# Kernel tuning notes

Hardware: AMD Instinct MI355X
Metric: run time of the kernel (lower is better)

The kernel has to match this reference:

```python
import jax, jax.numpy as jnp
import numpy as np
from jax import lax

C_IN, C_OUT, H, W = 64, 128, 512, 512


def setup_inputs() -> dict:
    key = jax.random.key(0)
    k1, k2, k3, k4 = jax.random.split(key, 4)
    x = jax.random.normal(k1, (C_IN, H, W), dtype=jnp.float32)
    # Conv2d params (eqx default: kernel 3x3, bias used). Small init scale for stability.
    conv_w = jax.random.normal(k2, (C_OUT, C_IN, 3, 3), dtype=jnp.float32) * 0.05
    conv_b = jax.random.normal(k3, (C_OUT,), dtype=jnp.float32) * 0.05
    fft_mask = jax.random.normal(k4, (C_OUT, H, W), dtype=jnp.float32)
    return {"x": x, "conv_w": conv_w, "conv_b": conv_b, "fft_mask": fft_mask}


def reference(x, conv_w, conv_b, fft_mask):
    # 3x3 same-padding conv on a single (C,H,W) sample -> (C_OUT,H,W)
    y = lax.conv_general_dilated(
        x[None],  # (1,C_IN,H,W)
        conv_w,
        window_strides=(1, 1),
        padding=((1, 1), (1, 1)),
        dimension_numbers=("NCHW", "OIHW", "NCHW"),
    )[0] + conv_b[:, None, None]
    # Per-channel spectral filter: FFT over (H,W), elementwise complex-mask
    # multiply, inverse FFT, take real part. Vectorized over channels.
    Y = jnp.fft.fftn(y, axes=(1, 2)) * fft_mask
    return jnp.fft.ifftn(Y, axes=(1, 2)).real
```

## Files before the change

### kernel.cpp

```cpp
#include <hip/hip_runtime.h>

#define CIN   64
#define COUT  128
#define HH    512
#define WW    512
#define HW    (HH*WW)

typedef __attribute__((ext_vector_type(8))) short  short8;
typedef __attribute__((ext_vector_type(4))) float  floatx4;


__device__ __forceinline__ unsigned short f2bf(float f) {
    unsigned u = __float_as_uint(f);
    u += 0x7fffu + ((u >> 16) & 1u);
    return (unsigned short)(u >> 16);
}

__device__ __forceinline__ void wave_sync() {
    __builtin_amdgcn_wave_barrier();
    asm volatile("s_waitcnt lgkmcnt(0)" ::: "memory");
    __builtin_amdgcn_sched_barrier(0);
}
template<bool BLK> __device__ __forceinline__ void xsync() {
    if (BLK) __syncthreads(); else wave_sync();
}


__global__ __launch_bounds__(256) void k_wprep(
        const float* __restrict__ cw,
        unsigned short* __restrict__ wt)
{
    int i = blockIdx.x * 256 + threadIdx.x;
    int tap = i >> 13;
    int co  = (i >> 6) & 127;
    int ci  = i & 63;
    wt[i] = f2bf(cw[(co * 64 + ci) * 9 + tap]);
}


__global__ __launch_bounds__(256) void k_xprep(
        const float* __restrict__ x,
        unsigned short* __restrict__ xt)
{
    __shared__ unsigned short tile[64][72];
    int t  = threadIdx.x;
    int h  = blockIdx.x >> 3;
    int w0 = (blockIdx.x & 7) << 6;
    int wl = t & 63;
#pragma unroll
    for (int it = 0; it < 16; ++it) {
        int ci = (t >> 6) + 4 * it;
        tile[wl][ci] = f2bf(x[ci * HW + h * 512 + w0 + wl]);
    }
    __syncthreads();
#pragma unroll
    for (int it = 0; it < 2; ++it) {
        int task = t + 256 * it;
        int w = task >> 3, seg = task & 7;
        *(short8*)&xt[((size_t)(h * 512 + w0 + w)) * 64 + seg * 8] =
            *(const short8*)&tile[w][seg * 8];
    }
}


__global__ __launch_bounds__(256) void k_maskT2(
        const float* __restrict__ mask,
        float* __restrict__ mt)
{
    __shared__ float t1[64][65];
    __shared__ float t2[64][65];
    int b  = blockIdx.x;
    int ch = b >> 6;
    int k0 = ((b >> 3) & 7) << 6;
    int c0 = (b & 7) << 6;
    int t  = threadIdx.x;
    int j  = t & 63, i0 = t >> 6;
    const float* mch = mask + (size_t)ch * HW;
#pragma unroll
    for (int it = 0; it < 16; ++it) {
        int i  = i0 + 4 * it;
        int mi = (512 - (k0 + i)) & 511;
        int mj = (512 - (c0 + j)) & 511;
        t1[i][j] = mch[(size_t)(k0 + i) * 512 + (c0 + j)];
        t2[i][j] = mch[(size_t)mi * 512 + mj];
    }
    __syncthreads();
    float* och = mt + (size_t)ch * HW;
#pragma unroll
    for (int it = 0; it < 16; ++it) {
        int jj = i0 + 4 * it;
        och[(size_t)(c0 + jj) * 512 + k0 + j] = t1[j][jj] + t2[j][jj];
    }
}


__global__ __launch_bounds__(512) void k_conv(
        const unsigned short* __restrict__ xt,
        const unsigned short* __restrict__ wt,
        const float* __restrict__ bias,
        float* __restrict__ y)
{
    __shared__ __align__(16) unsigned short As[3][130][68];

    int b  = blockIdx.x;
    int h  = b >> 2;
    int w0 = (b & 3) << 7;
    int t  = threadIdx.x;
    int lane = t & 63, wv = t >> 6;
    int wm = wv >> 2, wn = wv & 3;
    int l15 = lane & 15, quad = lane >> 4;

    for (int idx = t; idx < 3 * 130 * 8; idx += 512) {
        int dy  = idx / 1040;
        int rem = idx - dy * 1040;
        int p   = rem >> 3, seg = rem & 7;
        int hp  = h + dy - 1;
        int wq  = w0 - 1 + p;
        short8 v = {0, 0, 0, 0, 0, 0, 0, 0};
        if ((unsigned)hp < 512u && (unsigned)wq < 512u)
            v = *(const short8*)&xt[((size_t)(hp * 512 + wq)) * 64 + seg * 8];
        *(short8*)&As[dy][p][seg * 8] = v;
    }
    __syncthreads();

    floatx4 acc[4][2];
#pragma unroll
    for (int mt = 0; mt < 4; ++mt)
#pragma unroll
        for (int nt = 0; nt < 2; ++nt) {
            floatx4 z = {0.f, 0.f, 0.f, 0.f};
            acc[mt][nt] = z;
        }

#pragma unroll
    for (int tap = 0; tap < 9; ++tap) {
        int dy = tap / 3, dx = tap - dy * 3;
        short8 bfr[2][2];
#pragma unroll
        for (int nt = 0; nt < 2; ++nt)
#pragma unroll
            for (int kc = 0; kc < 2; ++kc) {
                int co = wn * 32 + nt * 16 + l15;
                bfr[nt][kc] = *(const short8*)
                    &wt[(tap * 128 + co) * 64 + kc * 32 + quad * 8];
            }
#pragma unroll
        for (int kc = 0; kc < 2; ++kc) {
            int c0 = kc * 32 + quad * 8;
            short8 afr[4];
#pragma unroll
            for (int mt = 0; mt < 4; ++mt) {
                int row = wm * 64 + mt * 16 + l15 + dx;
                afr[mt] = *(const short8*)&As[dy][row][c0];
            }
#pragma unroll
            for (int mt = 0; mt < 4; ++mt)
#pragma unroll
                for (int nt = 0; nt < 2; ++nt)
                    acc[mt][nt] = __builtin_amdgcn_mfma_f32_16x16x32_bf16(
                        afr[mt], bfr[nt][kc], acc[mt][nt], 0, 0, 0);
        }
    }

#pragma unroll
    for (int nt = 0; nt < 2; ++nt) {
        int co = wn * 32 + nt * 16 + l15;
        float bv = bias[co];
#pragma unroll
        for (int mt = 0; mt < 4; ++mt) {
            floatx4 o = acc[mt][nt];
            o[0] += bv; o[1] += bv; o[2] += bv; o[3] += bv;
            int m = wm * 64 + mt * 16 + quad * 4;
            *(floatx4*)&y[co * HW + h * 512 + w0 + m] = o;
        }
    }
}


#define FS 576

__device__ __forceinline__ int slotf(int c, int a) {
    return c * FS + ((a + (a >> 3)) ^ c);
}
__device__ __forceinline__ int dr6(int v) {
    return (v >> 3) + 8 * (v & 7);
}

__device__ __forceinline__ float2 cadd(float2 a, float2 b){ return make_float2(a.x+b.x, a.y+b.y); }
__device__ __forceinline__ float2 csub(float2 a, float2 b){ return make_float2(a.x-b.x, a.y-b.y); }

template<int DIR> __device__ __forceinline__ float2 twmul(float2 a, float2 t){
    return (DIR > 0) ? make_float2(a.x*t.x - a.y*t.y, a.x*t.y + a.y*t.x)
                     : make_float2(a.x*t.x + a.y*t.y, a.y*t.x - a.x*t.y);
}
template<int DIR> __device__ __forceinline__ float2 mulJ(float2 a){
    return (DIR > 0) ? make_float2(a.y, -a.x) : make_float2(-a.y, a.x);
}

#define RSQRT2 0.70710678118654752f

template<int DIR> __device__ __forceinline__ void dft8(float2* x){
    float2 a0 = cadd(x[0], x[4]), b0 = csub(x[0], x[4]);
    float2 a1 = cadd(x[1], x[5]), b1 = csub(x[1], x[5]);
    float2 a2 = cadd(x[2], x[6]), b2 = csub(x[2], x[6]);
    float2 a3 = cadd(x[3], x[7]), b3 = csub(x[3], x[7]);
    b1 = (DIR > 0) ? make_float2((b1.x + b1.y)*RSQRT2, (b1.y - b1.x)*RSQRT2)
                   : make_float2((b1.x - b1.y)*RSQRT2, (b1.y + b1.x)*RSQRT2);
    b2 = mulJ<DIR>(b2);
    b3 = (DIR > 0) ? make_float2((b3.y - b3.x)*RSQRT2, -(b3.x + b3.y)*RSQRT2)
                   : make_float2(-(b3.x + b3.y)*RSQRT2, (b3.x - b3.y)*RSQRT2);
    float2 c0 = cadd(a0, a2), d0 = csub(a0, a2);
    float2 c1 = cadd(a1, a3), d1 = mulJ<DIR>(csub(a1, a3));
    x[0] = cadd(c0, c1); x[4] = csub(c0, c1);
    x[2] = cadd(d0, d1); x[6] = csub(d0, d1);
    float2 e0 = cadd(b0, b2), f0 = csub(b0, b2);
    float2 e1 = cadd(b1, b3), f1 = mulJ<DIR>(csub(b1, b3));
    x[1] = cadd(e0, e1); x[5] = csub(e0, e1);
    x[3] = cadd(f0, f1); x[7] = csub(f0, f1);
}

template<bool BLK>
__device__ __forceinline__ void fft512_fwd(float2 X[2][8], float2* buf,
                                           const float2* tw, int w, int c) {
#pragma unroll
    for (int b = 0; b < 2; ++b) {
        dft8<1>(X[b]);
        int g = w + 32*b;
#pragma unroll
        for (int k = 1; k < 8; ++k) X[b][k] = twmul<1>(X[b][k], tw[g*k]);
    }
#pragma unroll
    for (int b = 0; b < 2; ++b) {
        int g = w + 32*b;
#pragma unroll
        for (int k = 0; k < 8; ++k) buf[slotf(c, k*64 + g)] = X[b][k];
    }
    xsync<BLK>();
#pragma unroll
    for (int b = 0; b < 2; ++b) {
        int u = w + 32*b; int bs = (u >> 3)*64 + (u & 7);
#pragma unroll
        for (int g2 = 0; g2 < 8; ++g2) X[b][g2] = buf[slotf(c, bs + 8*g2)];
    }
#pragma unroll
    for (int b = 0; b < 2; ++b) {
        dft8<1>(X[b]);
        int g1 = (w + 32*b) & 7;
#pragma unroll
        for (int k = 1; k < 8; ++k) X[b][k] = twmul<1>(X[b][k], tw[8*g1*k]);
    }
    xsync<BLK>();
#pragma unroll
    for (int b = 0; b < 2; ++b) {
        int u = w + 32*b; int bs = (u >> 3)*64 + (u & 7);
#pragma unroll
        for (int k = 0; k < 8; ++k) buf[slotf(c, bs + 8*k)] = X[b][k];
    }
    xsync<BLK>();
#pragma unroll
    for (int b = 0; b < 2; ++b) {
        int v = w + 32*b;
#pragma unroll
        for (int g1 = 0; g1 < 8; ++g1) X[b][g1] = buf[slotf(c, 8*v + g1)];
    }
#pragma unroll
    for (int b = 0; b < 2; ++b) dft8<1>(X[b]);
}

template<bool BLK>
__device__ __forceinline__ void fft512_inv(float2 X[2][8], float2* buf,
                                           const float2* tw, int w, int c) {
#pragma unroll
    for (int b = 0; b < 2; ++b) dft8<-1>(X[b]);
    xsync<BLK>();
#pragma unroll
    for (int b = 0; b < 2; ++b) {
        int v = w + 32*b;
#pragma unroll
        for (int g1 = 0; g1 < 8; ++g1) buf[slotf(c, 8*v + g1)] = X[b][g1];
    }
    xsync<BLK>();
#pragma unroll
    for (int b = 0; b < 2; ++b) {
        int u = w + 32*b; int bs = (u >> 3)*64 + (u & 7);
#pragma unroll
        for (int k = 0; k < 8; ++k) X[b][k] = buf[slotf(c, bs + 8*k)];
    }
#pragma unroll
    for (int b = 0; b < 2; ++b) {
        int g1 = (w + 32*b) & 7;
#pragma unroll
        for (int k = 1; k < 8; ++k) X[b][k] = twmul<-1>(X[b][k], tw[8*g1*k]);
        dft8<-1>(X[b]);
    }
    xsync<BLK>();
#pragma unroll
    for (int b = 0; b < 2; ++b) {
        int u = w + 32*b; int bs = (u >> 3)*64 + (u & 7);
#pragma unroll
        for (int g2 = 0; g2 < 8; ++g2) buf[slotf(c, bs + 8*g2)] = X[b][g2];
    }
    xsync<BLK>();
#pragma unroll
    for (int b = 0; b < 2; ++b) {
        int g = w + 32*b;
#pragma unroll
        for (int k = 0; k < 8; ++k) X[b][k] = buf[slotf(c, k*64 + g)];
    }
#pragma unroll
    for (int b = 0; b < 2; ++b) {
        int g = w + 32*b;
#pragma unroll
        for (int k = 1; k < 8; ++k) X[b][k] = twmul<-1>(X[b][k], tw[g*k]);
        dft8<-1>(X[b]);
    }
}

template<int NT>
__device__ __forceinline__ void build_tw(float2* tw, int t) {
    const float a0 = -6.283185307179586f / 512.0f;
#pragma unroll
    for (int i = 0; i < 512/NT; ++i) {
        float s, c;
        __sincosf(a0 * (float)(t + NT*i), &s, &c);
        tw[t + NT*i] = make_float2(c, s);
    }
}


__global__ __launch_bounds__(512) void k_rows_fwd_pair(
        const float* __restrict__ y,
        float2* __restrict__ Z)
{
    __shared__ float2 buf[16 * FS];
    __shared__ float2 tw[512];
    int t = threadIdx.x;
    build_tw<512>(tw, t);
    int c = t >> 5, w = t & 31;
    int p = blockIdx.x >> 5, r0 = (blockIdx.x & 31) << 4;
    const float* yA = y + (size_t)(2*p) * HW + (size_t)(r0 + c) * 512;
    const float* yB = yA + HW;

    float2 X[2][8];
#pragma unroll
    for (int b = 0; b < 2; ++b)
#pragma unroll
        for (int r = 0; r < 8; ++r) {
            int off = w + 32*b + 64*r;
            X[b][r] = make_float2(yA[off], yB[off]);
        }
    __syncthreads();
    fft512_fwd<false>(X, buf, tw, w, c);

    wave_sync();
#pragma unroll
    for (int b = 0; b < 2; ++b) {
        int kb = dr6(w + 32*b);
#pragma unroll
        for (int m = 0; m < 8; ++m) buf[slotf(c, kb + 64*m)] = X[b][m];
    }
    __syncthreads();
    size_t zb = (size_t)p * HW + r0;
    for (int it = 0; it < 16; ++it) {
        int n = t + 512*it;
        int col = n >> 4, rr = n & 15;
        Z[zb + (size_t)col*512 + rr] = buf[slotf(rr, col)];
    }
}

__device__ __forceinline__ int col_of(int g, int j) {
    if (g == 0) return (j < 4) ? j : (j == 4 ? 256 : 504 + j);
    return (j < 4) ? 4*g + j : 512 - 4*g - 7 + j;
}
__device__ __forceinline__ int jmir(int g, int j) {
    return (g == 0) ? ((8 - j) & 7) : (7 - j);
}

__global__ __launch_bounds__(256, 4) void k_cols_pair(
        float2* __restrict__ Z,
        const float* __restrict__ mt)
{
    __shared__ float2 buf[8 * FS];
    __shared__ float2 tw[512];
    int t = threadIdx.x;
    build_tw<256>(tw, t);
    int c = t >> 5, w = t & 31;
    int p = blockIdx.x >> 6, g = blockIdx.x & 63;
    int colc = col_of(g, c);
    int cm   = jmir(g, c);
    size_t zch = (size_t)p * HW;
    const float* mAp = mt + (size_t)(2*p) * HW + (size_t)colc * 512;
    const float* mBp = mAp + HW;

    for (int it = 0; it < 16; ++it) {
        int n = t + 256*it;
        int cj = n >> 9, row = n & 511;
        buf[slotf(cj, row)] = Z[zch + (size_t)col_of(g, cj)*512 + row];
    }
    float Sa[2][8], Sb[2][8];
#pragma unroll
    for (int b = 0; b < 2; ++b) {
        int kb = dr6(w + 32*b);
#pragma unroll
        for (int m = 0; m < 8; ++m) {
            int k1 = kb + 64*m;
            Sa[b][m] = mAp[k1];
            Sb[b][m] = mBp[k1];
        }
    }
    __syncthreads();

    float2 X[2][8];
#pragma unroll
    for (int b = 0; b < 2; ++b)
#pragma unroll
        for (int r = 0; r < 8; ++r)
            X[b][r] = buf[slotf(c, w + 32*b + 64*r)];
    wave_sync();
    fft512_fwd<false>(X, buf, tw, w, c);

    wave_sync();
#pragma unroll
    for (int b = 0; b < 2; ++b) {
        int kb = dr6(w + 32*b);
#pragma unroll
        for (int m = 0; m < 8; ++m) buf[slotf(c, kb + 64*m)] = X[b][m];
    }
    __syncthreads();

    const float s4 = 0.25f / 262144.0f;
#pragma unroll
    for (int b = 0; b < 2; ++b) {
        int kb = dr6(w + 32*b);
#pragma unroll
        for (int m = 0; m < 8; ++m) {
            int k1  = kb + 64*m;
            int mk1 = (512 - k1) & 511;
            float2 P = X[b][m];
            float2 Q = buf[slotf(cm, mk1)];
            float alpha = (Sa[b][m] + Sb[b][m]) * s4;
            float beta  = (Sa[b][m] - Sb[b][m]) * s4;
            X[b][m] = make_float2(alpha * P.x + beta * Q.x,
                                  alpha * P.y - beta * Q.y);
        }
    }
    __syncthreads();
    fft512_inv<false>(X, buf, tw, w, c);
    wave_sync();
#pragma unroll
    for (int b = 0; b < 2; ++b)
#pragma unroll
        for (int r = 0; r < 8; ++r)
            buf[slotf(c, w + 32*b + 64*r)] = X[b][r];
    __syncthreads();
    for (int it = 0; it < 16; ++it) {
        int n = t + 256*it;
        int cj = n >> 9, row = n & 511;
        Z[zch + (size_t)col_of(g, cj)*512 + row] = buf[slotf(cj, row)];
    }
}

__global__ __launch_bounds__(512) void k_rows_inv_pair(
        const float2* __restrict__ Z,
        float* __restrict__ out)
{
    __shared__ float2 buf[16 * FS];
    __shared__ float2 tw[512];
    int t = threadIdx.x;
    build_tw<512>(tw, t);
    int c = t >> 5, w = t & 31;
    int p = blockIdx.x >> 5, r0 = (blockIdx.x & 31) << 4;
    size_t zb = (size_t)p * HW + r0;

    for (int it = 0; it < 16; ++it) {
        int n = t + 512*it;
        int col = n >> 4, rr = n & 15;
        buf[slotf(rr, col)] = Z[zb + (size_t)col*512 + rr];
    }
    __syncthreads();

    float2 X[2][8];
#pragma unroll
    for (int b = 0; b < 2; ++b) {
        int kb = dr6(w + 32*b);
#pragma unroll
        for (int m = 0; m < 8; ++m) X[b][m] = buf[slotf(c, kb + 64*m)];
    }
    fft512_inv<false>(X, buf, tw, w, c);

    float* oA = out + (size_t)(2*p) * HW + (size_t)(r0 + c) * 512;
    float* oB = oA + HW;
#pragma unroll
    for (int b = 0; b < 2; ++b)
#pragma unroll
        for (int r = 0; r < 8; ++r) {
            int off = w + 32*b + 64*r;
            oA[off] = X[b][r].x;
            oB[off] = X[b][r].y;
        }
}


extern "C" void kernel_launch(void* const* d_in, const int* in_sizes, int n_in,
                              void* d_out, int out_size, void* d_ws, size_t ws_size,
                              hipStream_t stream) {
    const float* x    = (const float*)d_in[0];
    const float* cw   = (const float*)d_in[1];
    const float* cb   = (const float*)d_in[2];
    const float* mask = (const float*)d_in[3];

    float*  outRe = (float*)d_out;
    float2* ZT    = (float2*)d_ws;

    unsigned short* xt = (unsigned short*)d_ws;
    unsigned short* wt = (unsigned short*)d_ws + (size_t)HW * 64;

    k_wprep<<<288, 256, 0, stream>>>(cw, wt);
    k_xprep<<<4096, 256, 0, stream>>>(x, xt);
    k_conv<<<2048, 512, 0, stream>>>(xt, wt, cb, outRe);
    k_rows_fwd_pair<<<2048, 512, 0, stream>>>(outRe, ZT);
    k_maskT2<<<8192, 256, 0, stream>>>(mask, outRe);
    k_cols_pair<<<4096, 256, 0, stream>>>(ZT, outRe);
    k_rows_inv_pair<<<2048, 512, 0, stream>>>(ZT, outRe);
}
```

Baseline: 683.7 us.

## Pair-permute column storage and precompute packed mask alpha/beta coefficients

The mask preparation kernel now folds each channel pair's masks into packed (alpha, beta) float2 coefficients. These are written in the exact per-thread order the column FFT kernel reads, so that kernel does coalesced contiguous loads and skips the per-element add/scale. The spectrum columns are stored in a mirrored-pair permutation (posf), so each column block reads and writes one contiguous 8-column slab instead of gathering scattered columns. The row kernels pay a computed column index in exchange, and the mask kernel now reads the mask twice per channel and writes a float2 buffer into the output array.

```diff
diff --git a/kernel.cpp b/kernel.cpp
--- a/kernel.cpp
+++ b/kernel.cpp
@@ -25,6 +25,14 @@
     if (BLK) __syncthreads(); else wave_sync();
 }
 
+__device__ __forceinline__ int posf(int col) {
+    return (col == 0) ? 0 : (col == 256) ? 1
+         : (col < 256) ? 2*col : 2*(512 - col) + 1;
+}
+__device__ __forceinline__ int dr6(int v) {
+    return (v >> 3) + 8 * (v & 7);
+}
+
 
 __global__ __launch_bounds__(256) void k_wprep(
         const float* __restrict__ cw,
@@ -63,33 +71,43 @@
 }
 
 
-__global__ __launch_bounds__(256) void k_maskT2(
+__global__ __launch_bounds__(256) void k_AB(
         const float* __restrict__ mask,
-        float* __restrict__ mt)
-{
-    __shared__ float t1[64][65];
-    __shared__ float t2[64][65];
-    int b  = blockIdx.x;
-    int ch = b >> 6;
-    int k0 = ((b >> 3) & 7) << 6;
-    int c0 = (b & 7) << 6;
-    int t  = threadIdx.x;
-    int j  = t & 63, i0 = t >> 6;
-    const float* mch = mask + (size_t)ch * HW;
+        float2* __restrict__ ab)
+{
+    __shared__ float SA[64][65];
+    __shared__ float SB[64][65];
+    int blk = blockIdx.x;
+    int p  = blk >> 6;
+    int m  = (blk >> 3) & 7;
+    int ct = blk & 7;
+    int k0 = m << 6, c0 = ct << 6;
+    int t = threadIdx.x;
+    int j = t & 63, i0 = t >> 6;
+    const float* mA = mask + (size_t)(2*p) * HW;
+    const float* mB = mA + HW;
+    int mj = (512 - (c0 + j)) & 511;
 #pragma unroll
     for (int it = 0; it < 16; ++it) {
-        int i  = i0 + 4 * it;
-        int mi = (512 - (k0 + i)) & 511;
-        int mj = (512 - (c0 + j)) & 511;
-        t1[i][j] = mch[(size_t)(k0 + i) * 512 + (c0 + j)];
-        t2[i][j] = mch[(size_t)mi * 512 + mj];
-    }
-    __syncthreads();
-    float* och = mt + (size_t)ch * HW;
-#pragma unroll
-    for (int it = 0; it < 16; ++it) {
-        int jj = i0 + 4 * it;
-        och[(size_t)(c0 + jj) * 512 + k0 + j] = t1[j][jj] + t2[j][jj];
+        int i  = i0 + 4*it;
+        int k1 = k0 + i;
+        int mi = (512 - k1) & 511;
+        SA[i][j] = mA[(size_t)k1*512 + c0 + j] + mA[(size_t)mi*512 + mj];
+        SB[i][j] = mB[(size_t)k1*512 + c0 + j] + mB[(size_t)mi*512 + mj];
+    }
+    __syncthreads();
+    const float s4 = 0.25f / 262144.0f;
+    int w = t & 31, jb = t >> 5;
+#pragma unroll
+    for (int pass = 0; pass < 8; ++pass) {
+        int jj = jb + 8*pass;
+        size_t base = ((size_t)p*512 + posf(c0 + jj))*512;
+#pragma unroll
+        for (int b = 0; b < 2; ++b) {
+            int i = dr6(w + 32*b);
+            float sa = SA[i][jj], sb = SB[i][jj];
+            ab[base + (8*b + m)*32 + w] = make_float2((sa+sb)*s4, (sa-sb)*s4);
+        }
     }
 }
 
@@ -181,9 +199,6 @@
 
 __device__ __forceinline__ int slotf(int c, int a) {
     return c * FS + ((a + (a >> 3)) ^ c);
-}
-__device__ __forceinline__ int dr6(int v) {
-    return (v >> 3) + 8 * (v & 7);
 }
 
 __device__ __forceinline__ float2 cadd(float2 a, float2 b){ return make_float2(a.x+b.x, a.y+b.y); }
@@ -364,21 +379,13 @@
     for (int it = 0; it < 16; ++it) {
         int n = t + 512*it;
         int col = n >> 4, rr = n & 15;
-        Z[zb + (size_t)col*512 + rr] = buf[slotf(rr, col)];
-    }
-}
-
-__device__ __forceinline__ int col_of(int g, int j) {
-    if (g == 0) return (j < 4) ? j : (j == 4 ? 256 : 504 + j);
-    return (j < 4) ? 4*g + j : 512 - 4*g - 7 + j;
-}
-__device__ __forceinline__ int jmir(int g, int j) {
-    return (g == 0) ? ((8 - j) & 7) : (7 - j);
+        Z[zb + (size_t)posf(col)*512 + rr] = buf[slotf(rr, col)];
+    }
 }
 
 __global__ __launch_bounds__(256, 4) void k_cols_pair(
         float2* __restrict__ Z,
-        const float* __restrict__ mt)
+        const float2* __restrict__ ab)
 {
     __shared__ float2 buf[8 * FS];
     __shared__ float2 tw[512];
@@ -386,28 +393,20 @@
     build_tw<256>(tw, t);
     int c = t >> 5, w = t & 31;
     int p = blockIdx.x >> 6, g = blockIdx.x & 63;
-    int colc = col_of(g, c);
-    int cm   = jmir(g, c);
-    size_t zch = (size_t)p * HW;
-    const float* mAp = mt + (size_t)(2*p) * HW + (size_t)colc * 512;
-    const float* mBp = mAp + HW;
+    int cm = (g == 0 && c < 2) ? c : (c ^ 1);
+    size_t zblk = (size_t)p * HW + (size_t)(8*g) * 512;
+    const float2* abp = ab + ((size_t)p*512 + 8*g + c)*512;
 
     for (int it = 0; it < 16; ++it) {
         int n = t + 256*it;
-        int cj = n >> 9, row = n & 511;
-        buf[slotf(cj, row)] = Z[zch + (size_t)col_of(g, cj)*512 + row];
-    }
-    float Sa[2][8], Sb[2][8];
-#pragma unroll
-    for (int b = 0; b < 2; ++b) {
-        int kb = dr6(w + 32*b);
-#pragma unroll
-        for (int m = 0; m < 8; ++m) {
-            int k1 = kb + 64*m;
-            Sa[b][m] = mAp[k1];
-            Sb[b][m] = mBp[k1];
-        }
-    }
+        buf[slotf(n >> 9, n & 511)] = Z[zblk + n];
+    }
+    float2 AB[2][8];
+#pragma unroll
+    for (int b = 0; b < 2; ++b)
+#pragma unroll
+        for (int m = 0; m < 8; ++m)
+            AB[b][m] = abp[(8*b + m)*32 + w];
     __syncthreads();
 
     float2 X[2][8];
@@ -428,7 +427,6 @@
     }
     __syncthreads();
 
-    const float s4 = 0.25f / 262144.0f;
 #pragma unroll
     for (int b = 0; b < 2; ++b) {
         int kb = dr6(w + 32*b);
@@ -438,8 +436,7 @@
             int mk1 = (512 - k1) & 511;
             float2 P = X[b][m];
             float2 Q = buf[slotf(cm, mk1)];
-            float alpha = (Sa[b][m] + Sb[b][m]) * s4;
-            float beta  = (Sa[b][m] - Sb[b][m]) * s4;
+            float alpha = AB[b][m].x, beta = AB[b][m].y;
             X[b][m] = make_float2(alpha * P.x + beta * Q.x,
                                   alpha * P.y - beta * Q.y);
         }
@@ -455,8 +452,7 @@
     __syncthreads();
     for (int it = 0; it < 16; ++it) {
         int n = t + 256*it;
-        int cj = n >> 9, row = n & 511;
-        Z[zch + (size_t)col_of(g, cj)*512 + row] = buf[slotf(cj, row)];
+        Z[zblk + n] = buf[slotf(n >> 9, n & 511)];
     }
 }
 
@@ -475,7 +471,7 @@
     for (int it = 0; it < 16; ++it) {
         int n = t + 512*it;
         int col = n >> 4, rr = n & 15;
-        buf[slotf(rr, col)] = Z[zb + (size_t)col*512 + rr];
+        buf[slotf(rr, col)] = Z[zb + (size_t)posf(col)*512 + rr];
     }
     __syncthreads();
 
@@ -510,7 +506,8 @@
     const float* mask = (const float*)d_in[3];
 
     float*  outRe = (float*)d_out;
-    float2* ZT    = (float2*)d_ws;
+    float2* ZTP   = (float2*)d_ws;
+    float2* AB    = (float2*)d_out;
 
     unsigned short* xt = (unsigned short*)d_ws;
     unsigned short* wt = (unsigned short*)d_ws + (size_t)HW * 64;
@@ -518,8 +515,8 @@
     k_wprep<<<288, 256, 0, stream>>>(cw, wt);
     k_xprep<<<4096, 256, 0, stream>>>(x, xt);
     k_conv<<<2048, 512, 0, stream>>>(xt, wt, cb, outRe);
-    k_rows_fwd_pair<<<2048, 512, 0, stream>>>(outRe, ZT);
-    k_maskT2<<<8192, 256, 0, stream>>>(mask, outRe);
-    k_cols_pair<<<4096, 256, 0, stream>>>(ZT, outRe);
-    k_rows_inv_pair<<<2048, 512, 0, stream>>>(ZT, outRe);
-}
+    k_rows_fwd_pair<<<2048, 512, 0, stream>>>(outRe, ZTP);
+    k_AB<<<4096, 256, 0, stream>>>(mask, AB);
+    k_cols_pair<<<4096, 256, 0, stream>>>(ZTP, AB);
+    k_rows_inv_pair<<<2048, 512, 0, stream>>>(ZTP, outRe);
+}
```

Result: slower. 767.6 us (+12.3%).
